# Performance work log

Measured on AMD Instinct MI355X. Metric: run time of the kernel, lower is better.

Reference implementation:

```python
import jax, jax.numpy as jnp
import numpy as np

T = 64        # time steps (batch)
N_SIDE = 256  # grid side, N = N_SIDE**2 flattened grid points
HID = 32      # hidden width of the shared per-point MLP
IN_CH = 5     # 5-point periodic stencil (l, l2, center, r, r2)


def _stencil_gather(x, n):
    """Replicates MLPConv._preprocess / make_px / get_value exactly.

    x: [T, n*n] flattened periodic grid. Returns [T, n*n, 5].
    get_value wraps indices via the piecewise rule (v-n if v>=n) and relies on
    numpy negative flat indexing for v=-1, which is the final `% (n*n)` here.
    Output position i_loop*n + j_loop reads grid flat index (j_loop+ik) + n*(i_loop+jk).
    """
    ii = jnp.arange(n)[:, None]  # i_loop (outer loop in make_px)
    jj = jnp.arange(n)[None, :]  # j_loop (inner loop)

    def idx(ik, jk):
        a = jj + ik
        a = jnp.where(a >= n, a - n, a)
        b = ii + jk
        b = jnp.where(b >= n, b - n, b)
        return ((a + n * b) % (n * n)).reshape(-1)  # [n*n]

    # channel order from _preprocess: cat([l, l2, px, r, r2], -1)
    offsets = [(-1, 0), (0, -1), (0, 0), (1, 0), (0, 1)]
    cols = jnp.stack([idx(ik, jk) for ik, jk in offsets], axis=-1)  # [n*n, 5]
    return x[:, cols]  # [T, n*n, 5]


def setup_inputs() -> dict:
    key = jax.random.key(0)
    ks = jax.random.split(key, 7)
    n2 = N_SIDE * N_SIDE
    x = jax.random.normal(ks[0], (T, n2), dtype=jnp.float32)
    # torch Linear weights are [out, in]; we store transposed [in, out] for x @ W.
    # Original init: xavier_normal * 10, bias zeros; scaled normals are equivalent for a baseline.
    def w(k, fan_in, fan_out):
        std = 10.0 * np.sqrt(2.0 / (fan_in + fan_out))
        return std * jax.random.normal(k, (fan_in, fan_out), dtype=jnp.float32)
    return {
        "x": x,
        "W0": w(ks[1], IN_CH, HID), "b0": jnp.zeros((HID,), jnp.float32),
        "W1": w(ks[2], HID, HID),   "b1": jnp.zeros((HID,), jnp.float32),
        "W2": w(ks[3], HID, 1),     "b2": jnp.zeros((1,), jnp.float32),
    }


def reference(x, W0, b0, W1, b1, W2, b2):
    # Note: the x_copy dual path in the torch forward never affects the returned
    # tensor (dead code), so the faithful math is a plain 3-layer MLP over the
    # 5-point periodic stencil gather, ELU between layers, no final activation.
    n = int(np.sqrt(x.shape[1]))
    px = _stencil_gather(x, n)                 # [T, N, 5]
    h = jax.nn.elu(px @ W0 + b0)               # [T, N, HID]
    h = jax.nn.elu(h @ W1 + b1)                # [T, N, HID]
    out = h @ W2 + b2                          # [T, N, 1]
    return out.squeeze(-1)                     # [T, N] (matches res.squeeze())
```

## Files before the change

kernel.cpp:

```cpp
#include <hip/hip_runtime.h>
#include <hip/hip_fp16.h>

#define NS 256
#define N2 (NS * NS)
#define HID 32
#define T_STEPS 64

typedef _Float16 h2     __attribute__((ext_vector_type(2)));
typedef _Float16 half8  __attribute__((ext_vector_type(8)));
typedef float    float4v __attribute__((ext_vector_type(4)));

union H8 { half8 v8; h2 v2[4]; };

__device__ __forceinline__ h2 pk(float a, float b) {
    return __builtin_bit_cast(h2, __builtin_amdgcn_cvt_pkrtz(a, b));
}

__device__ __forceinline__ h2 elu2(h2 z) {
    h2 zero; zero[0] = (_Float16)0.f; zero[1] = (_Float16)0.f;
    h2 zm  = __builtin_elementwise_min(z, zero);
    h2 e   = __builtin_elementwise_exp2(zm * (_Float16)1.442695041f);
    h2 em1 = e + (_Float16)(-1.0f);
    return __builtin_elementwise_max(z, em1);
}

__global__ __launch_bounds__(256, 4) void mlpconv_pipe4_kernel(
    const float* __restrict__ x,
    const float* __restrict__ W0, const float* __restrict__ b0,
    const float* __restrict__ W1, const float* __restrict__ b1,
    const float* __restrict__ W2, const float* __restrict__ b2,
    float* __restrict__ out)
{
    const int lane = threadIdx.x & 63;
    const int m    = lane & 15;
    const int kg   = lane >> 4;

    const int c0 = 8 * (m >> 2) + (m & 3);
    const int c1 = c0 + 4;

    H8 a00, a01;
    #pragma unroll
    for (int i = 0; i < 8; ++i) {
        const int k = 8 * kg + i;
        a00.v8[i] = (k < 5) ? (_Float16)W0[k * HID + c0] : (_Float16)0.f;
        a01.v8[i] = (k < 5) ? (_Float16)W0[k * HID + c1] : (_Float16)0.f;
    }
    H8 a10, a11;
    #pragma unroll
    for (int i = 0; i < 8; ++i) {
        a10.v8[i] = (_Float16)W1[(8 * kg + i) * HID + c0];
        a11.v8[i] = (_Float16)W1[(8 * kg + i) * HID + c1];
    }
    H8 a2;
    #pragma unroll
    for (int i = 0; i < 8; ++i)
        a2.v8[i] = (m == 0) ? (_Float16)W2[8 * kg + i] : (_Float16)0.f;

    float4v cl0a, cl0b, cl1a, cl1b;
    #pragma unroll
    for (int r = 0; r < 4; ++r) {
        cl0a[r] = b0[8 * kg + r];
        cl0b[r] = b0[8 * kg + 4 + r];
        cl1a[r] = b1[8 * kg + r];
        cl1b[r] = b1[8 * kg + 4 + r];
    }
    float4v c2;
    c2[0] = (kg == 0) ? b2[0] : 0.0f;
    c2[1] = 0.0f; c2[2] = 0.0f; c2[3] = 0.0f;

    asm volatile("" : "+v"(a00.v8), "+v"(a01.v8), "+v"(a10.v8), "+v"(a11.v8),
                      "+v"(a2.v8), "+v"(cl0a), "+v"(cl0b), "+v"(cl1a), "+v"(cl1b));

    const int wid   = __builtin_amdgcn_readfirstlane(threadIdx.x >> 6);
    const int t     = blockIdx.y;
    const int i0    = blockIdx.x * 4 + wid;
    const int sbase = i0 << 8;

    const float* __restrict__ xt  = x + ((size_t)t << 16);
    const float* __restrict__ xtu = xt + ((i0 == 0)      ? (N2 - NS) : -NS);
    const float* __restrict__ xtd = xt + ((i0 == NS - 1) ? -(N2 - NS) : NS);
    float* __restrict__       ob  = out + ((size_t)t << 16);

    const unsigned vc0 = (unsigned)(sbase + m);
    const unsigned vl0 = (unsigned)(sbase + m - 1);
    const unsigned vlA = (sbase + m == 0) ? (unsigned)(N2 - 1) : vl0;
    const unsigned vr0 = (unsigned)(sbase + m + 1);
    const unsigned vrF = (m == 15) ? (unsigned)sbase : (vr0 + 240u);

    #define LOADS(l, dst)                                                \
    {                                                                    \
        const unsigned o = 16u * (unsigned)(l);                          \
        dst[0] = xt [((l) == 0)  ? vlA : (vl0 + o)];                     \
        dst[1] = xtu[vc0 + o];                                           \
        dst[2] = xt [vc0 + o];                                           \
        dst[3] = xt [((l) == 15) ? vrF : (vr0 + o)];                     \
        dst[4] = xtd[vc0 + o];                                           \
    }

    float in[4][5];
    float res[16];

    LOADS(0, in[0])
    LOADS(1, in[1])
    LOADS(2, in[2])

    #pragma unroll
    for (int l = 0; l < 16; ++l) {
        if (l + 3 < 16) LOADS(l + 3, in[(l + 3) % 4])

        const float* s = in[l % 4];

        H8 bf;
        bf.v2[0] = pk(s[0], s[1]);
        bf.v2[1] = pk(s[2], s[3]);
        bf.v2[2] = pk(s[4], s[4]);
        bf.v2[3] = bf.v2[2];

        float4v d0 = __builtin_amdgcn_mfma_f32_16x16x32_f16(a00.v8, bf.v8, cl0a, 0, 0, 0);
        float4v d1 = __builtin_amdgcn_mfma_f32_16x16x32_f16(a01.v8, bf.v8, cl0b, 0, 0, 0);

        H8 hf;
        hf.v2[0] = elu2(pk(d0[0], d0[1]));
        hf.v2[1] = elu2(pk(d0[2], d0[3]));
        hf.v2[2] = elu2(pk(d1[0], d1[1]));
        hf.v2[3] = elu2(pk(d1[2], d1[3]));

        float4v e0 = __builtin_amdgcn_mfma_f32_16x16x32_f16(a10.v8, hf.v8, cl1a, 0, 0, 0);
        float4v e1 = __builtin_amdgcn_mfma_f32_16x16x32_f16(a11.v8, hf.v8, cl1b, 0, 0, 0);

        H8 gf;
        gf.v2[0] = elu2(pk(e0[0], e0[1]));
        gf.v2[1] = elu2(pk(e0[2], e0[3]));
        gf.v2[2] = elu2(pk(e1[0], e1[1]));
        gf.v2[3] = elu2(pk(e1[2], e1[3]));

        float4v dz = __builtin_amdgcn_mfma_f32_16x16x32_f16(a2.v8, gf.v8, c2, 0, 0, 0);

        res[l] = dz[0];
    }
    #undef LOADS

    if (kg == 0) {
        #pragma unroll
        for (int l = 0; l < 16; ++l)
            ob[vc0 + 16u * (unsigned)l] = res[l];
    }
}

extern "C" void kernel_launch(void* const* d_in, const int* in_sizes, int n_in,
                              void* d_out, int out_size, void* d_ws, size_t ws_size,
                              hipStream_t stream) {
    const float* x  = (const float*)d_in[0];
    const float* W0 = (const float*)d_in[1];
    const float* b0 = (const float*)d_in[2];
    const float* W1 = (const float*)d_in[3];
    const float* b1 = (const float*)d_in[4];
    const float* W2 = (const float*)d_in[5];
    const float* b2 = (const float*)d_in[6];
    float* out = (float*)d_out;

    dim3 grid(NS / 4, T_STEPS);
    mlpconv_pipe4_kernel<<<grid, dim3(256), 0, stream>>>(
        x, W0, b0, W1, b1, W2, b2, out);
}
```

Measured before the change: 128.8 us.

## Stage stencil rows in LDS instead of per-lane global gathers

Each block now cooperatively loads the six grid rows it needs (one halo row above and below its four rows) into shared memory, syncs, and then reads all five stencil taps from LDS. This replaces five overlapping global loads per point, and the software prefetch ring, with one coalesced global load per element plus cheap LDS reads. Periodic wrap is handled by the row indexing at load time and by pointer tricks for the left and right edges. It adds a block barrier and 6 KB of LDS per block, and raises the launch-bounds occupancy hint from 4 to 6, which may constrain registers.

```diff
diff --git a/kernel.cpp b/kernel.cpp
--- a/kernel.cpp
+++ b/kernel.cpp
@@ -24,14 +24,17 @@
     return __builtin_elementwise_max(z, em1);
 }
 
-__global__ __launch_bounds__(256, 4) void mlpconv_pipe4_kernel(
+__global__ __launch_bounds__(256, 6) void mlpconv_lds_kernel(
     const float* __restrict__ x,
     const float* __restrict__ W0, const float* __restrict__ b0,
     const float* __restrict__ W1, const float* __restrict__ b1,
     const float* __restrict__ W2, const float* __restrict__ b2,
     float* __restrict__ out)
 {
-    const int lane = threadIdx.x & 63;
+    __shared__ float lds[6 * NS];
+
+    const int tid  = threadIdx.x;
+    const int lane = tid & 63;
     const int m    = lane & 15;
     const int kg   = lane >> 4;
 
@@ -71,49 +74,40 @@
     asm volatile("" : "+v"(a00.v8), "+v"(a01.v8), "+v"(a10.v8), "+v"(a11.v8),
                       "+v"(a2.v8), "+v"(cl0a), "+v"(cl0b), "+v"(cl1a), "+v"(cl1b));
 
-    const int wid   = __builtin_amdgcn_readfirstlane(threadIdx.x >> 6);
-    const int t     = blockIdx.y;
-    const int i0    = blockIdx.x * 4 + wid;
+    const int t    = blockIdx.y;
+    const int i0b  = blockIdx.x * 4;
+    const float* __restrict__ xt = x   + ((size_t)t << 16);
+    float* __restrict__       ob = out + ((size_t)t << 16);
+
+    #pragma unroll
+    for (int it = 0; it < 6; ++it) {
+        const int gr = (i0b + 255 + it) & 255;
+        lds[it * NS + tid] = xt[(gr << 8) | tid];
+    }
+    __syncthreads();
+
+    const int wid = __builtin_amdgcn_readfirstlane(tid >> 6);
+    const int i0  = i0b + wid;
     const int sbase = i0 << 8;
 
-    const float* __restrict__ xt  = x + ((size_t)t << 16);
-    const float* __restrict__ xtu = xt + ((i0 == 0)      ? (N2 - NS) : -NS);
-    const float* __restrict__ xtd = xt + ((i0 == NS - 1) ? -(N2 - NS) : NS);
-    float* __restrict__       ob  = out + ((size_t)t << 16);
+    const float* vp = &lds[wid * NS + m];
+    const float* vpR = (m == 15) ? &lds[(wid + 1) * NS] : (vp + 256 + 1 + 240);
 
-    const unsigned vc0 = (unsigned)(sbase + m);
-    const unsigned vl0 = (unsigned)(sbase + m - 1);
-    const unsigned vlA = (sbase + m == 0) ? (unsigned)(N2 - 1) : vl0;
-    const unsigned vr0 = (unsigned)(sbase + m + 1);
-    const unsigned vrF = (m == 15) ? (unsigned)sbase : (vr0 + 240u);
-
-    #define LOADS(l, dst)                                                \
-    {                                                                    \
-        const unsigned o = 16u * (unsigned)(l);                          \
-        dst[0] = xt [((l) == 0)  ? vlA : (vl0 + o)];                     \
-        dst[1] = xtu[vc0 + o];                                           \
-        dst[2] = xt [vc0 + o];                                           \
-        dst[3] = xt [((l) == 15) ? vrF : (vr0 + o)];                     \
-        dst[4] = xtd[vc0 + o];                                           \
-    }
-
-    float in[4][5];
     float res[16];
-
-    LOADS(0, in[0])
-    LOADS(1, in[1])
-    LOADS(2, in[2])
 
     #pragma unroll
     for (int l = 0; l < 16; ++l) {
-        if (l + 3 < 16) LOADS(l + 3, in[(l + 3) % 4])
-
-        const float* s = in[l % 4];
+        const int o = 16 * l;
+        const float s0 = vp[256 + o - 1];
+        const float s1 = vp[o];
+        const float s2 = vp[256 + o];
+        const float s3 = (l == 15) ? *vpR : vp[256 + o + 1];
+        const float s4 = vp[512 + o];
 
         H8 bf;
-        bf.v2[0] = pk(s[0], s[1]);
-        bf.v2[1] = pk(s[2], s[3]);
-        bf.v2[2] = pk(s[4], s[4]);
+        bf.v2[0] = pk(s0, s1);
+        bf.v2[1] = pk(s2, s3);
+        bf.v2[2] = pk(s4, s4);
         bf.v2[3] = bf.v2[2];
 
         float4v d0 = __builtin_amdgcn_mfma_f32_16x16x32_f16(a00.v8, bf.v8, cl0a, 0, 0, 0);
@@ -138,9 +132,9 @@
 
         res[l] = dz[0];
     }
-    #undef LOADS
 
     if (kg == 0) {
+        const unsigned vc0 = (unsigned)(sbase + m);
         #pragma unroll
         for (int l = 0; l < 16; ++l)
             ob[vc0 + 16u * (unsigned)l] = res[l];
@@ -160,6 +154,6 @@
     float* out = (float*)d_out;
 
     dim3 grid(NS / 4, T_STEPS);
-    mlpconv_pipe4_kernel<<<grid, dim3(256), 0, stream>>>(
+    mlpconv_lds_kernel<<<grid, dim3(256), 0, stream>>>(
         x, W0, b0, W1, b1, W2, b2, out);
 }
```

New measurement: 134.1 us. 1.04x slower.
